# Kernel tuning notes

Hardware: AMD Instinct MI355X
Metric: run time of the kernel (lower is better)

## Reference

```python
import jax, jax.numpy as jnp
import numpy as np

D = 1024
NH = 16
HD = D // NH
DFF = 4 * D
EPS = 1e-5


def setup_inputs() -> dict:
    key = jax.random.key(0)
    ks = jax.random.split(key, 12)
    s = lambda fan_in: 1.0 / np.sqrt(fan_in)
    return {
        "x": jax.random.normal(ks[0], (2, 2048, D), dtype=jnp.float32),
        # weights stored [in, out] (transpose of torch Linear layout)
        "w_qkv": jax.random.uniform(ks[1], (D, 3 * D), minval=-s(D), maxval=s(D)),
        "w_proj": jax.random.uniform(ks[2], (D, D), minval=-s(D), maxval=s(D)),
        "ln1_w": jnp.ones((D,), jnp.float32),
        "ln1_b": jnp.zeros((D,), jnp.float32),
        "ln2_w": jnp.ones((D,), jnp.float32),
        "ln2_b": jnp.zeros((D,), jnp.float32),
        "fc1_w": jax.random.uniform(ks[3], (D, DFF), minval=-s(D), maxval=s(D)),
        "fc1_b": jax.random.uniform(ks[4], (DFF,), minval=-s(D), maxval=s(D)),
        "fc2_w": jax.random.uniform(ks[5], (DFF, D), minval=-s(DFF), maxval=s(DFF)),
        "fc2_b": jax.random.uniform(ks[6], (D,), minval=-s(DFF), maxval=s(DFF)),
    }


def _layernorm(x, w, b):
    mu = jnp.mean(x, axis=-1, keepdims=True)
    var = jnp.mean(jnp.square(x - mu), axis=-1, keepdims=True)
    return (x - mu) * jax.lax.rsqrt(var + EPS) * w + b


def _attn(x, w_qkv, w_proj):
    B, T, C = x.shape
    qkv = x @ w_qkv  # [B,T,3C]
    q, k, v = jnp.split(qkv, 3, axis=-1)
    q = q.reshape(B, T, NH, HD).transpose(0, 2, 1, 3)  # [B,nh,T,hd]
    k = k.reshape(B, T, NH, HD).transpose(0, 2, 1, 3)
    v = v.reshape(B, T, NH, HD).transpose(0, 2, 1, 3)
    att = jnp.einsum("bhqd,bhkd->bhqk", q, k) / np.sqrt(HD)
    causal = jnp.tril(jnp.ones((T, T), bool))
    att = jnp.where(causal, att, -jnp.inf)
    att = jax.nn.softmax(att, axis=-1)
    out = jnp.einsum("bhqk,bhkd->bhqd", att, v)
    out = out.transpose(0, 2, 1, 3).reshape(B, T, C)
    return out @ w_proj


def reference(x, w_qkv, w_proj, ln1_w, ln1_b, ln2_w, ln2_b, fc1_w, fc1_b, fc2_w, fc2_b):
    x = x + _attn(_layernorm(x, ln1_w, ln1_b), w_qkv, w_proj)
    h = _layernorm(x, ln2_w, ln2_b)
    h = jax.nn.gelu(h @ fc1_w + fc1_b, approximate=False) @ fc2_w + fc2_b
    return x + h
```

## Files before the change

### kernel.cpp

```cpp
#include <hip/hip_runtime.h>


typedef short  bf16x8 __attribute__((ext_vector_type(8)));
typedef short  bf16x4 __attribute__((ext_vector_type(4)));
typedef float  fx4    __attribute__((ext_vector_type(4)));

#define DEV static __device__ __forceinline__

DEV short f2bf(float f) {
    unsigned u = __builtin_bit_cast(unsigned, f);
    u += 0x7fffu + ((u >> 16) & 1u);
    return (short)(u >> 16);
}

template <int CTRL> DEV float dppmax(float v) {
    int x = __builtin_amdgcn_update_dpp(0, __builtin_bit_cast(int, v), CTRL, 0xF, 0xF, true);
    return fmaxf(v, __builtin_bit_cast(float, x));
}
template <int CTRL> DEV float dppadd(float v) {
    int x = __builtin_amdgcn_update_dpp(0, __builtin_bit_cast(int, v), CTRL, 0xF, 0xF, true);
    return v + __builtin_bit_cast(float, x);
}
DEV float rowmax16(float v) {
    v = dppmax<0x121>(v); v = dppmax<0x122>(v); v = dppmax<0x124>(v); v = dppmax<0x128>(v);
    return v;
}
DEV float rowsum16(float v) {
    v = dppadd<0x121>(v); v = dppadd<0x122>(v); v = dppadd<0x124>(v); v = dppadd<0x128>(v);
    return v;
}

#define AS1(p) ((__attribute__((address_space(1))) void*)(p))
#define AS3(p) ((__attribute__((address_space(3))) void*)(p))

__global__ __launch_bounds__(256) void ln_kernel(const float* __restrict__ x,
                                                 const float* __restrict__ w,
                                                 const float* __restrict__ b,
                                                 short* __restrict__ out)
{
    int row = blockIdx.x;
    int tid = threadIdx.x;
    const float4 v = *(const float4*)(x + (size_t)row * 1024 + tid * 4);
    float s = v.x + v.y + v.z + v.w;
    float q = v.x * v.x + v.y * v.y + v.z * v.z + v.w * v.w;
#pragma unroll
    for (int off = 32; off > 0; off >>= 1) {
        s += __shfl_down(s, off);
        q += __shfl_down(q, off);
    }
    __shared__ float ls[4], lq[4];
    if ((tid & 63) == 0) { ls[tid >> 6] = s; lq[tid >> 6] = q; }
    __syncthreads();
    float S  = ls[0] + ls[1] + ls[2] + ls[3];
    float Q  = lq[0] + lq[1] + lq[2] + lq[3];
    float mu  = S * (1.0f / 1024.0f);
    float var = Q * (1.0f / 1024.0f) - mu * mu;
    float inv = rsqrtf(var + 1e-5f);
    float4 wv = *(const float4*)(w + tid * 4);
    float4 bv = *(const float4*)(b + tid * 4);
    bf16x4 o;
    o[0] = f2bf((v.x - mu) * inv * wv.x + bv.x);
    o[1] = f2bf((v.y - mu) * inv * wv.y + bv.y);
    o[2] = f2bf((v.z - mu) * inv * wv.z + bv.z);
    o[3] = f2bf((v.w - mu) * inv * wv.w + bv.w);
    *(bf16x4*)(out + (size_t)row * 1024 + tid * 4) = o;
}

__global__ void transpose_f32_bf16(const float* __restrict__ in,
                                   short* __restrict__ out, int R, int C)
{
    __shared__ float tile[32][33];
    int c0 = blockIdx.x * 32, r0 = blockIdx.y * 32;
    int tx = threadIdx.x, ty = threadIdx.y;
#pragma unroll
    for (int dy = 0; dy < 32; dy += 8)
        tile[ty + dy][tx] = in[(size_t)(r0 + ty + dy) * C + c0 + tx];
    __syncthreads();
#pragma unroll
    for (int dy = 0; dy < 32; dy += 8)
        out[(size_t)(c0 + ty + dy) * R + r0 + tx] = f2bf(tile[tx][ty + dy]);
}

__global__ void vt_extract(const short* __restrict__ qkv, short* __restrict__ vt)
{
    __shared__ short tile[32][33];
    int t0 = blockIdx.x * 32, d0 = blockIdx.y * 32;
    int bh = blockIdx.z;
    int tx = threadIdx.x, ty = threadIdx.y;
    size_t inbase  = (size_t)(bh >> 4) * 2048 * 3072 + 2048 + (bh & 15) * 64;
    size_t outbase = (size_t)bh * 64 * 2048;
#pragma unroll
    for (int dy = 0; dy < 32; dy += 8)
        tile[ty + dy][tx] = qkv[inbase + (size_t)(t0 + ty + dy) * 3072 + d0 + tx];
    __syncthreads();
#pragma unroll
    for (int dy = 0; dy < 32; dy += 8)
        vt[outbase + (size_t)(d0 + ty + dy) * 2048 + t0 + tx] = tile[tx][ty + dy];
}

template <int BN, bool BIAS, bool GELU, bool RESID, bool OUT_BF16>
__global__ __launch_bounds__(256) void gemm_bt(const short* __restrict__ A,
                                               const short* __restrict__ Bt,
                                               void* __restrict__ Cout,
                                               const float* __restrict__ bias,
                                               const float* __restrict__ resid,
                                               int M, int N, int K)
{
    constexpr int NJ = BN / 32;
    __shared__ short As[128 * 32];
    __shared__ short Bs[BN * 32];
    int tid  = threadIdx.x;
    int lane = tid & 63, wv = tid >> 6;
    int quad = lane >> 4, l15 = lane & 15;
    int m0 = blockIdx.y * 128, n0 = blockIdx.x * BN;
    int wr = (wv >> 1) * 64, wc = (wv & 1) * (BN / 2);
    fx4 acc[4][NJ] = {};
    int srow = lane >> 2;
    int scol = (lane & 3) * 8;
    const short* Ab = A  + (size_t)m0 * K;
    const short* Bb = Bt + (size_t)n0 * K;

    for (int k0 = 0; k0 < K; k0 += 32) {
#pragma unroll
        for (int c = wv; c < 8; c += 4) {
            int row = c * 16 + srow;
            __builtin_amdgcn_global_load_lds(AS1(Ab + (size_t)row * K + k0 + scol),
                                             AS3(&As[c * 512]), 16, 0, 0);
        }
#pragma unroll
        for (int c = wv; c < BN / 16; c += 4) {
            int row = c * 16 + srow;
            __builtin_amdgcn_global_load_lds(AS1(Bb + (size_t)row * K + k0 + scol),
                                             AS3(&Bs[c * 512]), 16, 0, 0);
        }
        __syncthreads();
        bf16x8 af[4], bfr[NJ];
#pragma unroll
        for (int i = 0; i < 4; ++i)
            af[i] = *(const bf16x8*)&As[(wr + i * 16 + l15) * 32 + quad * 8];
#pragma unroll
        for (int j = 0; j < NJ; ++j)
            bfr[j] = *(const bf16x8*)&Bs[(wc + j * 16 + l15) * 32 + quad * 8];
#pragma unroll
        for (int i = 0; i < 4; ++i)
#pragma unroll
            for (int j = 0; j < NJ; ++j)
                acc[i][j] = __builtin_amdgcn_mfma_f32_16x16x32_bf16(af[i], bfr[j], acc[i][j], 0, 0, 0);
        __syncthreads();
    }

#pragma unroll
    for (int i = 0; i < 4; ++i) {
#pragma unroll
        for (int j = 0; j < NJ; ++j) {
#pragma unroll
            for (int r = 0; r < 4; ++r) {
                int row = m0 + wr + i * 16 + quad * 4 + r;
                int col = n0 + wc + j * 16 + l15;
                float v = acc[i][j][r];
                if constexpr (BIAS)  v += bias[col];
                if constexpr (GELU)  v = 0.5f * v * (1.0f + erff(v * 0.70710678118654752f));
                if constexpr (RESID) v += resid[(size_t)row * N + col];
                if constexpr (OUT_BF16) ((short*)Cout)[(size_t)row * N + col] = f2bf(v);
                else                    ((float*)Cout)[(size_t)row * N + col] = v;
            }
        }
    }
}

__global__ __launch_bounds__(256) void attn_kernel(const short* __restrict__ qkv,
                                                   const short* __restrict__ vt,
                                                   short* __restrict__ out)
{
    __shared__ short Ks[2][64 * 64];
    __shared__ short Vs[2][64 * 64];
    __shared__ short Ps[4 * 16 * 64];
    const float CS = 0.125f * 1.44269504088896f;
    int tid  = threadIdx.x, lane = tid & 63, wv = tid >> 6;
    int quad = lane >> 4, l15 = lane & 15;
    int b = blockIdx.z, h = blockIdx.y, j = blockIdx.x;

    const size_t kbase = (size_t)b * 2048 * 3072 + 1024 + h * 64;
    const size_t vbase = (size_t)(b * 16 + h) * 64 * 2048;
    int srow = lane >> 3;
    int sg   = lane & 7;
    int scol = (sg ^ srow) * 8;
    int rg0  = (quad ^ (l15 & 7)) * 8;

    for (int item = 0; item < 2; ++item) {
        int qt = item ? j : 31 - j;
        int q0 = qt * 64;

        bf16x8 qf[2];
#pragma unroll
        for (int ks = 0; ks < 2; ++ks)
            qf[ks] = *(const bf16x8*)&qkv[(size_t)(b * 2048 + q0 + wv * 16 + l15) * 3072
                                           + h * 64 + ks * 32 + quad * 8];
        float mi[4], li[4];
        fx4 oacc[4] = {};
#pragma unroll
        for (int r = 0; r < 4; ++r) { mi[r] = -1e30f; li[r] = 0.0f; }

#pragma unroll
        for (int c = wv; c < 8; c += 4) {
            int row = c * 8 + srow;
            __builtin_amdgcn_global_load_lds(AS1(qkv + kbase + (size_t)row * 3072 + scol),
                                             AS3(&Ks[0][c * 512]), 16, 0, 0);
            __builtin_amdgcn_global_load_lds(AS1(vt + vbase + (size_t)row * 2048 + scol),
                                             AS3(&Vs[0][c * 512]), 16, 0, 0);
        }
        __syncthreads();

        for (int kt = 0; kt <= qt; ++kt) {
            int cur = kt & 1;
            if (kt < qt) {
                int nb = cur ^ 1;
                int tn = (kt + 1) * 64;
#pragma unroll
                for (int c = wv; c < 8; c += 4) {
                    int row = c * 8 + srow;
                    __builtin_amdgcn_global_load_lds(AS1(qkv + kbase + (size_t)(tn + row) * 3072 + scol),
                                                     AS3(&Ks[nb][c * 512]), 16, 0, 0);
                    __builtin_amdgcn_global_load_lds(AS1(vt + vbase + (size_t)row * 2048 + tn + scol),
                                                     AS3(&Vs[nb][c * 512]), 16, 0, 0);
                }
            }

            fx4 s[4];
#pragma unroll
            for (int nt = 0; nt < 4; ++nt) {
                bf16x8 kf0 = *(const bf16x8*)&Ks[cur][(nt * 16 + l15) * 64 + rg0];
                bf16x8 kf1 = *(const bf16x8*)&Ks[cur][(nt * 16 + l15) * 64 + (rg0 ^ 32)];
                fx4 z = {0.f, 0.f, 0.f, 0.f};
                z = __builtin_amdgcn_mfma_f32_16x16x32_bf16(qf[0], kf0, z, 0, 0, 0);
                z = __builtin_amdgcn_mfma_f32_16x16x32_bf16(qf[1], kf1, z, 0, 0, 0);
                s[nt] = z;
            }
            if (kt == qt) {
#pragma unroll
                for (int nt = 0; nt < 4; ++nt)
#pragma unroll
                    for (int r = 0; r < 4; ++r)
                        if (nt * 16 + l15 > wv * 16 + quad * 4 + r) s[nt][r] = -1e30f;
            }

            float mnew[4], alpha[4], rsum[4];
#pragma unroll
            for (int r = 0; r < 4; ++r) {
                float v = fmaxf(fmaxf(s[0][r], s[1][r]), fmaxf(s[2][r], s[3][r]));
                v = rowmax16(v);
                mnew[r]  = fmaxf(mi[r], v);
                alpha[r] = exp2f((mi[r] - mnew[r]) * CS);
                mi[r] = mnew[r];
                rsum[r] = 0.0f;
            }
#pragma unroll
            for (int nt = 0; nt < 4; ++nt)
#pragma unroll
                for (int r = 0; r < 4; ++r) {
                    float p = exp2f((s[nt][r] - mnew[r]) * CS);
                    rsum[r] += p;
                    int rr = quad * 4 + r;
                    int col = nt * 16 + l15;
                    int g = (col >> 3) ^ (rr & 7);
                    Ps[wv * 1024 + rr * 64 + g * 8 + (col & 7)] = f2bf(p);
                }
#pragma unroll
            for (int r = 0; r < 4; ++r) {
                float v = rowsum16(rsum[r]);
                li[r] = li[r] * alpha[r] + v;
#pragma unroll
                for (int dt = 0; dt < 4; ++dt) oacc[dt][r] *= alpha[r];
            }

            bf16x8 pf0 = *(const bf16x8*)&Ps[wv * 1024 + l15 * 64 + rg0];
            bf16x8 pf1 = *(const bf16x8*)&Ps[wv * 1024 + l15 * 64 + (rg0 ^ 32)];
#pragma unroll
            for (int dt = 0; dt < 4; ++dt) {
                bf16x8 vf0 = *(const bf16x8*)&Vs[cur][(dt * 16 + l15) * 64 + rg0];
                bf16x8 vf1 = *(const bf16x8*)&Vs[cur][(dt * 16 + l15) * 64 + (rg0 ^ 32)];
                oacc[dt] = __builtin_amdgcn_mfma_f32_16x16x32_bf16(pf0, vf0, oacc[dt], 0, 0, 0);
                oacc[dt] = __builtin_amdgcn_mfma_f32_16x16x32_bf16(pf1, vf1, oacc[dt], 0, 0, 0);
            }
            __syncthreads();
        }

        float inv[4];
#pragma unroll
        for (int r = 0; r < 4; ++r) inv[r] = 1.0f / li[r];
#pragma unroll
        for (int dt = 0; dt < 4; ++dt)
#pragma unroll
            for (int r = 0; r < 4; ++r) {
                int row = q0 + wv * 16 + quad * 4 + r;
                int col = h * 64 + dt * 16 + l15;
                out[((size_t)b * 2048 + row) * 1024 + col] = f2bf(oacc[dt][r] * inv[r]);
            }
    }
}

extern "C" void kernel_launch(void* const* d_in, const int* in_sizes, int n_in,
                              void* d_out, int out_size, void* d_ws, size_t ws_size,
                              hipStream_t stream)
{
    const float* x      = (const float*)d_in[0];
    const float* w_qkv  = (const float*)d_in[1];
    const float* w_proj = (const float*)d_in[2];
    const float* ln1_w  = (const float*)d_in[3];
    const float* ln1_b  = (const float*)d_in[4];
    const float* ln2_w  = (const float*)d_in[5];
    const float* ln2_b  = (const float*)d_in[6];
    const float* fc1_w  = (const float*)d_in[7];
    const float* fc1_b  = (const float*)d_in[8];
    const float* fc2_w  = (const float*)d_in[9];
    const float* fc2_b  = (const float*)d_in[10];
    float* out = (float*)d_out;
    char*  ws  = (char*)d_ws;

    size_t off = 0;
    auto alloc = [&](size_t bytes) { void* p = ws + off; off += (bytes + 255) & ~(size_t)255; return p; };
    short* tw_qkv  = (short*)alloc((size_t)3072 * 1024 * 2);
    short* tw_proj = (short*)alloc((size_t)1024 * 1024 * 2);
    short* tfc1    = (short*)alloc((size_t)4096 * 1024 * 2);
    short* tfc2    = (short*)alloc((size_t)1024 * 4096 * 2);
    short* xn      = (short*)alloc((size_t)4096 * 1024 * 2);
    short* qkvb    = (short*)alloc((size_t)4096 * 3072 * 2);
    short* vtb     = (short*)alloc((size_t)32 * 64 * 2048 * 2);
    short* attnb   = (short*)alloc((size_t)4096 * 1024 * 2);
    float* x1      = (float*)alloc((size_t)4096 * 1024 * 4);
    short* h1      = qkvb;

    dim3 tb(32, 8);
    transpose_f32_bf16<<<dim3(3072 / 32, 1024 / 32), tb, 0, stream>>>(w_qkv, tw_qkv, 1024, 3072);
    transpose_f32_bf16<<<dim3(1024 / 32, 1024 / 32), tb, 0, stream>>>(w_proj, tw_proj, 1024, 1024);
    transpose_f32_bf16<<<dim3(4096 / 32, 1024 / 32), tb, 0, stream>>>(fc1_w, tfc1, 1024, 4096);
    transpose_f32_bf16<<<dim3(1024 / 32, 4096 / 32), tb, 0, stream>>>(fc2_w, tfc2, 4096, 1024);

    ln_kernel<<<4096, 256, 0, stream>>>(x, ln1_w, ln1_b, xn);
    gemm_bt<128, false, false, false, true><<<dim3(3072 / 128, 4096 / 128), 256, 0, stream>>>(
        xn, tw_qkv, qkvb, nullptr, nullptr, 4096, 3072, 1024);
    vt_extract<<<dim3(2048 / 32, 64 / 32, 32), tb, 0, stream>>>(qkvb, vtb);
    attn_kernel<<<dim3(16, 16, 2), 256, 0, stream>>>(qkvb, vtb, attnb);
    gemm_bt<64, false, false, true, false><<<dim3(1024 / 64, 4096 / 128), 256, 0, stream>>>(
        attnb, tw_proj, x1, nullptr, x, 4096, 1024, 1024);
    ln_kernel<<<4096, 256, 0, stream>>>(x1, ln2_w, ln2_b, xn);
    gemm_bt<128, true, true, false, true><<<dim3(4096 / 128, 4096 / 128), 256, 0, stream>>>(
        xn, tfc1, h1, fc1_b, nullptr, 4096, 4096, 1024);
    gemm_bt<64, true, false, true, false><<<dim3(1024 / 64, 4096 / 128), 256, 0, stream>>>(
        h1, tfc2, out, fc2_b, x1, 4096, 1024, 4096);
}
```

Before: 408.7 us.

## Double-buffer GEMM LDS tiles, swizzle LDS layout, split-K the N=1024 GEMMs

```diff
diff --git a/kernel.cpp b/kernel.cpp
--- a/kernel.cpp
+++ b/kernel.cpp
@@ -98,49 +98,60 @@
         vt[outbase + (size_t)(d0 + ty + dy) * 2048 + t0 + tx] = tile[tx][ty + dy];
 }
 
-template <int BN, bool BIAS, bool GELU, bool RESID, bool OUT_BF16>
+template <int BN, bool BIAS, bool GELU, bool RESID, bool OUT_BF16, bool PARTIAL>
 __global__ __launch_bounds__(256) void gemm_bt(const short* __restrict__ A,
                                                const short* __restrict__ Bt,
                                                void* __restrict__ Cout,
+                                               void* __restrict__ Cout2,
                                                const float* __restrict__ bias,
                                                const float* __restrict__ resid,
                                                int M, int N, int K)
 {
     constexpr int NJ = BN / 32;
-    __shared__ short As[128 * 32];
-    __shared__ short Bs[BN * 32];
+    __shared__ short As[2][128 * 32];
+    __shared__ short Bs[2][BN * 32];
     int tid  = threadIdx.x;
     int lane = tid & 63, wv = tid >> 6;
     int quad = lane >> 4, l15 = lane & 15;
     int m0 = blockIdx.y * 128, n0 = blockIdx.x * BN;
+    int SK   = gridDim.z;
+    int kbeg = blockIdx.z * (K / SK);
+    int NK   = (K / SK) / 32;
     int wr = (wv >> 1) * 64, wc = (wv & 1) * (BN / 2);
     fx4 acc[4][NJ] = {};
     int srow = lane >> 2;
-    int scol = (lane & 3) * 8;
+    int scol = ((lane & 3) ^ (srow & 3)) * 8;
+    int rg   = (quad ^ (l15 & 3)) * 8;
     const short* Ab = A  + (size_t)m0 * K;
     const short* Bb = Bt + (size_t)n0 * K;
 
-    for (int k0 = 0; k0 < K; k0 += 32) {
+    auto stage = [&](int buf, int k0) {
 #pragma unroll
         for (int c = wv; c < 8; c += 4) {
             int row = c * 16 + srow;
             __builtin_amdgcn_global_load_lds(AS1(Ab + (size_t)row * K + k0 + scol),
-                                             AS3(&As[c * 512]), 16, 0, 0);
+                                             AS3(&As[buf][c * 512]), 16, 0, 0);
         }
 #pragma unroll
         for (int c = wv; c < BN / 16; c += 4) {
             int row = c * 16 + srow;
             __builtin_amdgcn_global_load_lds(AS1(Bb + (size_t)row * K + k0 + scol),
-                                             AS3(&Bs[c * 512]), 16, 0, 0);
+                                             AS3(&Bs[buf][c * 512]), 16, 0, 0);
         }
-        __syncthreads();
+    };
+
+    stage(0, kbeg);
+    __syncthreads();
+    for (int kt = 0; kt < NK; ++kt) {
+        int cur = kt & 1;
+        if (kt + 1 < NK) stage(cur ^ 1, kbeg + (kt + 1) * 32);
         bf16x8 af[4], bfr[NJ];
 #pragma unroll
         for (int i = 0; i < 4; ++i)
-            af[i] = *(const bf16x8*)&As[(wr + i * 16 + l15) * 32 + quad * 8];
+            af[i] = *(const bf16x8*)&As[cur][(wr + i * 16 + l15) * 32 + rg];
 #pragma unroll
         for (int j = 0; j < NJ; ++j)
-            bfr[j] = *(const bf16x8*)&Bs[(wc + j * 16 + l15) * 32 + quad * 8];
+            bfr[j] = *(const bf16x8*)&Bs[cur][(wc + j * 16 + l15) * 32 + rg];
 #pragma unroll
         for (int i = 0; i < 4; ++i)
 #pragma unroll
@@ -149,23 +160,56 @@
         __syncthreads();
     }
 
-#pragma unroll
-    for (int i = 0; i < 4; ++i) {
-#pragma unroll
-        for (int j = 0; j < NJ; ++j) {
-#pragma unroll
-            for (int r = 0; r < 4; ++r) {
-                int row = m0 + wr + i * 16 + quad * 4 + r;
-                int col = n0 + wc + j * 16 + l15;
-                float v = acc[i][j][r];
-                if constexpr (BIAS)  v += bias[col];
-                if constexpr (GELU)  v = 0.5f * v * (1.0f + erff(v * 0.70710678118654752f));
-                if constexpr (RESID) v += resid[(size_t)row * N + col];
-                if constexpr (OUT_BF16) ((short*)Cout)[(size_t)row * N + col] = f2bf(v);
-                else                    ((float*)Cout)[(size_t)row * N + col] = v;
-            }
-        }
-    }
+    if constexpr (PARTIAL) {
+        float* P = blockIdx.z ? (float*)Cout2 : (float*)Cout;
+#pragma unroll
+        for (int i = 0; i < 4; ++i)
+#pragma unroll
+            for (int j = 0; j < NJ; ++j)
+#pragma unroll
+                for (int r = 0; r < 4; ++r) {
+                    int row = m0 + wr + i * 16 + quad * 4 + r;
+                    int col = n0 + wc + j * 16 + l15;
+                    P[(size_t)row * N + col] = acc[i][j][r];
+                }
+    } else {
+#pragma unroll
+        for (int i = 0; i < 4; ++i)
+#pragma unroll
+            for (int j = 0; j < NJ; ++j)
+#pragma unroll
+                for (int r = 0; r < 4; ++r) {
+                    int row = m0 + wr + i * 16 + quad * 4 + r;
+                    int col = n0 + wc + j * 16 + l15;
+                    float v = acc[i][j][r];
+                    if constexpr (BIAS)  v += bias[col];
+                    if constexpr (GELU)  v = 0.5f * v * (1.0f + erff(v * 0.70710678118654752f));
+                    if constexpr (RESID) v += resid[(size_t)row * N + col];
+                    if constexpr (OUT_BF16) ((short*)Cout)[(size_t)row * N + col] = f2bf(v);
+                    else                    ((float*)Cout)[(size_t)row * N + col] = v;
+                }
+    }
+}
+
+template <bool BIAS>
+__global__ __launch_bounds__(256) void reduce2(const float* __restrict__ p0,
+                                               const float* __restrict__ p1,
+                                               const float* __restrict__ resid,
+                                               const float* __restrict__ bias,
+                                               float* __restrict__ out, int N)
+{
+    size_t idx = ((size_t)blockIdx.x * 256 + threadIdx.x) * 4;
+    float4 a = *(const float4*)(p0 + idx);
+    float4 b = *(const float4*)(p1 + idx);
+    float4 r = *(const float4*)(resid + idx);
+    float4 v;
+    v.x = a.x + b.x + r.x; v.y = a.y + b.y + r.y;
+    v.z = a.z + b.z + r.z; v.w = a.w + b.w + r.w;
+    if constexpr (BIAS) {
+        const float4 bv = *(const float4*)(bias + (idx & (N - 1)));
+        v.x += bv.x; v.y += bv.y; v.z += bv.z; v.w += bv.w;
+    }
+    *(float4*)(out + idx) = v;
 }
 
 __global__ __launch_bounds__(256) void attn_kernel(const short* __restrict__ qkv,
@@ -328,6 +372,7 @@
     short* vtb     = (short*)alloc((size_t)32 * 64 * 2048 * 2);
     short* attnb   = (short*)alloc((size_t)4096 * 1024 * 2);
     float* x1      = (float*)alloc((size_t)4096 * 1024 * 4);
+    float* pk      = (float*)alloc((size_t)4096 * 1024 * 4);
     short* h1      = qkvb;
 
     dim3 tb(32, 8);
@@ -337,15 +382,17 @@
     transpose_f32_bf16<<<dim3(1024 / 32, 4096 / 32), tb, 0, stream>>>(fc2_w, tfc2, 4096, 1024);
 
     ln_kernel<<<4096, 256, 0, stream>>>(x, ln1_w, ln1_b, xn);
-    gemm_bt<128, false, false, false, true><<<dim3(3072 / 128, 4096 / 128), 256, 0, stream>>>(
-        xn, tw_qkv, qkvb, nullptr, nullptr, 4096, 3072, 1024);
+    gemm_bt<128, false, false, false, true, false><<<dim3(24, 32, 1), 256, 0, stream>>>(
+        xn, tw_qkv, qkvb, nullptr, nullptr, nullptr, 4096, 3072, 1024);
     vt_extract<<<dim3(2048 / 32, 64 / 32, 32), tb, 0, stream>>>(qkvb, vtb);
     attn_kernel<<<dim3(16, 16, 2), 256, 0, stream>>>(qkvb, vtb, attnb);
-    gemm_bt<64, false, false, true, false><<<dim3(1024 / 64, 4096 / 128), 256, 0, stream>>>(
-        attnb, tw_proj, x1, nullptr, x, 4096, 1024, 1024);
+    gemm_bt<64, false, false, false, false, true><<<dim3(16, 32, 2), 256, 0, stream>>>(
+        attnb, tw_proj, x1, pk, nullptr, nullptr, 4096, 1024, 1024);
+    reduce2<false><<<4096, 256, 0, stream>>>(x1, pk, x, nullptr, x1, 1024);
     ln_kernel<<<4096, 256, 0, stream>>>(x1, ln2_w, ln2_b, xn);
-    gemm_bt<128, true, true, false, true><<<dim3(4096 / 128, 4096 / 128), 256, 0, stream>>>(
-        xn, tfc1, h1, fc1_b, nullptr, 4096, 4096, 1024);
-    gemm_bt<64, true, false, true, false><<<dim3(1024 / 64, 4096 / 128), 256, 0, stream>>>(
-        h1, tfc2, out, fc2_b, x1, 4096, 1024, 4096);
-}
+    gemm_bt<128, true, true, false, true, false><<<dim3(32, 32, 1), 256, 0, stream>>>(
+        xn, tfc1, h1, nullptr, fc1_b, nullptr, 4096, 4096, 1024);
+    gemm_bt<64, false, false, false, false, true><<<dim3(16, 32, 2), 256, 0, stream>>>(
+        h1, tfc2, out, pk, nullptr, nullptr, 4096, 1024, 4096);
+    reduce2<true><<<4096, 256, 0, stream>>>(out, pk, x1, fc2_b, out, 1024);
+}
```

After: 397.5 us. 1.03x faster.
